# Optimization experiments

Hardware: AMD Instinct MI355X
Metric: run time of the kernel (lower is better)

The kernel has to match this reference:

```python
import math
import jax, jax.numpy as jnp
import numpy as np

# MrLoRA ranks: halving from highest_rank = total_rank//2 = 32 down to 1
RANKS = [32, 16, 8, 4, 2, 1]
TOTAL_R = sum(RANKS)  # 63
LORA_ALPHA = 16.0
IN_F, OUT_F = 4096, 4096
BATCH, SEQ = 4, 2048


def setup_inputs() -> dict:
    key = jax.random.key(0)
    k0, k1, k2, k3 = jax.random.split(key, 4)
    x = jax.random.normal(k0, (BATCH, SEQ, IN_F), dtype=jnp.float32)
    # Base linear layer (nn.Linear weight is [out, in], plus bias)
    W_base = jax.random.normal(k1, (OUT_F, IN_F), dtype=jnp.float32) * 0.02
    b_base = jnp.zeros((OUT_F,), dtype=jnp.float32)
    # Concatenated per-rank LoRA weights: A rows stacked -> [TOTAL_R, IN_F],
    # B cols stacked -> [OUT_F, TOTAL_R]. Mathematically identical to the
    # per-rank ModuleDict since the branch outputs are summed.
    A = jax.random.normal(k2, (TOTAL_R, IN_F), dtype=jnp.float32) / math.sqrt(IN_F)
    B = jax.random.normal(k3, (OUT_F, TOTAL_R), dtype=jnp.float32) * 0.02
    alphas = jnp.ones((len(RANKS),), dtype=jnp.float32)
    # use_rslora=True -> scaling = alpha / sqrt(r)
    scalings = jnp.array([LORA_ALPHA / math.sqrt(r) for r in RANKS], dtype=jnp.float32)
    return {"x": x, "W_base": W_base, "b_base": b_base, "A": A, "B": B,
            "alphas": alphas, "scalings": scalings}


def reference(x, W_base, b_base, A, B, alphas, scalings):
    # static map: row r of concatenated A belongs to which rank branch
    seg = np.repeat(np.arange(len(RANKS)), RANKS)  # [TOTAL_R]
    base = jnp.einsum('bsi,oi->bso', x, W_base) + b_base
    # dropout p=0 -> identity
    combined = (alphas * scalings)[seg]            # [TOTAL_R]
    z = jnp.einsum('bsi,ri->bsr', x, A) * combined # scaled low-rank projections
    adapter = jnp.einsum('bsr,or->bso', z, B)      # sum over all rank branches
    return base + adapter
```

## Files before the change

### kernel.cpp

```cpp
#include <hip/hip_runtime.h>
#include <hip/hip_fp16.h>
#include <cstdint>

#define IN_F 4096
#define OUT_F 4096
#define M_TOT 8192
#define TOTAL_R 63

typedef __attribute__((ext_vector_type(8))) _Float16 f16x8;
typedef __attribute__((ext_vector_type(4))) float f32x4;
typedef __attribute__((ext_vector_type(8))) unsigned short u16x8;
typedef __attribute__((ext_vector_type(4))) unsigned short u16x4;

__device__ __forceinline__ void gload_lds16(const void* g, void* l) {
  __builtin_amdgcn_global_load_lds((const __attribute__((address_space(1))) void*)g,
                                   (__attribute__((address_space(3))) void*)l,
                                   16, 0, 0);
}

__device__ __forceinline__ int seg_of(int r) {
  return (r < 32) ? 0 : (r < 48) ? 1 : (r < 56) ? 2 : (r < 60) ? 3 : (r < 62) ? 4 : 5;
}

__global__ __launch_bounds__(256) void prep_kernel(
    const float* __restrict__ x, const float* __restrict__ Wb,
    const float* __restrict__ A, const float* __restrict__ Bm,
    const float* __restrict__ alphas, const float* __restrict__ scalings,
    uint16_t* __restrict__ xh, uint16_t* __restrict__ wh) {
  __shared__ float sA[63 * 128];
  __shared__ float sCS[64];
  const int id = blockIdx.x;
  const int q9 = id / 9, rem = id % 9;
  const int t = threadIdx.x;

  if (rem != 8) {
    const int cid = q9 * 8 + rem;
    size_t i = (size_t)cid * 256 + t;
    const float4* xv = (const float4*)x;
    float4 v0 = xv[2 * i];
    float4 v1 = xv[2 * i + 1];
    float v[8] = {v0.x, v0.y, v0.z, v0.w, v1.x, v1.y, v1.z, v1.w};
    u16x8 h;
#pragma unroll
    for (int k = 0; k < 8; ++k) h[k] = __half_as_ushort(__float2half_rn(v[k]));
    *(u16x8*)(xh + 8 * i) = h;
    return;
  }

  const int mid = q9;
  const int o0 = (mid >> 5) * 64, i0 = (mid & 31) * 128;

  if (t < 64) {
    int r = t;
    sCS[t] = (r < TOTAL_R) ? alphas[seg_of(r)] * scalings[seg_of(r)] : 0.f;
  }
#pragma unroll
  for (int k = 0; k < 8; ++k) {
    int idx = k * 256 + t;
    if (idx < 63 * 32) {
      int r = idx >> 5, c = idx & 31;
      *(f32x4*)(sA + r * 128 + c * 4) =
          *(const f32x4*)(A + (size_t)r * IN_F + i0 + c * 4);
    }
  }
  __syncthreads();

  const int oo = t & 63, iq = t >> 6;
  const size_t ob = (size_t)(o0 + oo);
  const size_t obase = ob * IN_F + i0 + iq * 32;
  const float* bmrow = Bm + ob * TOTAL_R;
  f32x4 acc4[8];
#pragma unroll
  for (int v = 0; v < 8; ++v) acc4[v] = *(const f32x4*)(Wb + obase + v * 4);
#pragma unroll 9
  for (int r = 0; r < TOTAL_R; ++r) {
    const float coeff = bmrow[r] * sCS[r];
    const f32x4* ar = (const f32x4*)(sA + r * 128 + iq * 32);
#pragma unroll
    for (int v = 0; v < 8; ++v) acc4[v] += coeff * ar[v];
  }
#pragma unroll
  for (int v = 0; v < 8; ++v) {
    u16x4 h;
#pragma unroll
    for (int k = 0; k < 4; ++k) h[k] = __half_as_ushort(__float2half_rn(acc4[v][k]));
    *(u16x4*)(wh + obase + v * 4) = h;
  }
}

__global__ __launch_bounds__(512, 2) void gemm_mrlora(
    const uint16_t* __restrict__ xh, const uint16_t* __restrict__ wh,
    const float* __restrict__ bias, float* __restrict__ out) {
  __shared__ uint16_t lds[2][2][2][8192];
  const int t = threadIdx.x;
  const int l = t & 63;
  const int w = t >> 6;
  const int wm = w >> 2, wn = w & 3;
  const int lr = l & 15, lg = l >> 4;

  const int xcd = blockIdx.x & 7;
  const int kk = blockIdx.x >> 3;
  const int bm = xcd * 4 + (kk & 3);
  const int bn = kk >> 2;
  const size_t brow = (size_t)bm * 256;
  const size_t bcol = (size_t)bn * 256;

  const int sp = (t & 7) ^ ((t >> 3) & 7);
  const int grow = (t >> 3) * 2 + (sp >> 2);
  const int gcol = (sp & 3) * 8;
  const uint16_t* pX = xh + (brow + grow) * (size_t)IN_F + gcol;
  const uint16_t* pW = wh + (bcol + grow) * (size_t)IN_F + gcol;
  const int t8 = t * 8;

  int aoff[2][4], boff[4];
#pragma unroll
  for (int ih = 0; ih < 2; ++ih)
#pragma unroll
    for (int i2 = 0; i2 < 4; ++i2) {
      int row = wm * 128 + ih * 64 + i2 * 16 + lr;
      aoff[ih][i2] = (row >> 1) * 64 + (((((row & 1) << 2) | lg) ^ ((row >> 1) & 7)) << 3);
    }
#pragma unroll
  for (int j = 0; j < 4; ++j) {
    int row = wn * 64 + j * 16 + lr;
    boff[j] = (row >> 1) * 64 + (((((row & 1) << 2) | lg) ^ ((row >> 1) & 7)) << 3);
  }

  f32x4 acc[8][4] = {};
  f16x8 afr[4], bfr[4];

#define STG(NB, MAT, KS, KT)                                                   \
  do {                                                                         \
    const uint16_t* _s = ((MAT) ? pW : pX) + (KT) * 64 + (KS) * 32;            \
    gload_lds16(_s, &lds[NB][MAT][KS][t8]);                                    \
    gload_lds16(_s + 128 * (size_t)IN_F, &lds[NB][MAT][KS][t8 + 4096]);        \
  } while (0)

#define RDA(BUF, IH, KS)                                                       \
  _Pragma("unroll") for (int _i = 0; _i < 4; ++_i)                             \
      afr[_i] = *(const f16x8*)&lds[BUF][0][KS][aoff[IH][_i]];

#define RDB(BUF, KS)                                                           \
  _Pragma("unroll") for (int _j = 0; _j < 4; ++_j)                             \
      bfr[_j] = *(const f16x8*)&lds[BUF][1][KS][boff[_j]];

#define MM16(IH, KS)                                                           \
  do {                                                                         \
    __builtin_amdgcn_s_setprio(1);                                             \
    _Pragma("unroll") for (int _i = 0; _i < 4; ++_i)                           \
        _Pragma("unroll") for (int _j = 0; _j < 4; ++_j)                       \
            acc[(IH) * 4 + _i][_j] = __builtin_amdgcn_mfma_f32_16x16x32_f16(   \
                afr[_i], bfr[_j], acc[(IH) * 4 + _i][_j], 0, 0, 0);            \
    __builtin_amdgcn_s_setprio(0);                                             \
  } while (0)

#define BAR __builtin_amdgcn_s_barrier()

#define KTILE(BUF, KT, S2W, S4W, DOSTG)                                        \
  do {                                                                         \
                                                      \
    RDA(BUF, 0, 0); RDB(BUF, 0);                                               \
    if (DOSTG) STG(1 - (BUF), 0, 0, (KT) + 1);                                 \
    BAR;                                                                       \
    MM16(0, 0);                                                                \
    BAR;                                                                       \
                                             \
    RDA(BUF, 1, 0);                                                            \
    if (DOSTG) STG(1 - (BUF), 1, 0, (KT) + 1);                                 \
    BAR;                                                                       \
    MM16(1, 0);                                                                \
    asm volatile("s_waitcnt " S2W ::: "memory");  \
    BAR;                                                                       \
                                                      \
    RDA(BUF, 0, 1); RDB(BUF, 1);                                               \
    if (DOSTG) STG(1 - (BUF), 0, 1, (KT) + 1);                                 \
    BAR;                                                                       \
    MM16(0, 1);                                                                \
    BAR;                                                                       \
                                             \
    RDA(BUF, 1, 1);                                                            \
    if (DOSTG) STG(1 - (BUF), 1, 1, (KT) + 1);                                 \
    BAR;                                                                       \
    MM16(1, 1);                                                                \
    asm volatile("s_waitcnt " S4W ::: "memory");       \
    BAR;                                                                       \
  } while (0)

  STG(0, 0, 0, 0); STG(0, 1, 0, 0); STG(0, 0, 1, 0); STG(0, 1, 1, 0);
  asm volatile("s_waitcnt vmcnt(4)" ::: "memory");
  BAR;

#pragma unroll 1
  for (int tt = 0; tt < 31; ++tt) {
    KTILE(0, 2 * tt,     "vmcnt(4)", "vmcnt(4)", 1);
    KTILE(1, 2 * tt + 1, "vmcnt(4)", "vmcnt(4)", 1);
  }
  KTILE(0, 62, "vmcnt(4)", "vmcnt(4)", 1);
  KTILE(1, 63, "vmcnt(0)", "vmcnt(0)", 0);

#undef KTILE
#undef BAR
#undef MM16
#undef RDB
#undef RDA
#undef STG

#pragma unroll
  for (int j = 0; j < 4; ++j) {
    const size_t col = bcol + wn * 64 + j * 16 + lr;
    const float bs = bias[col];
#pragma unroll
    for (int i = 0; i < 8; ++i) {
      const size_t row0 = brow + wm * 128 + i * 16 + lg * 4;
#pragma unroll
      for (int r = 0; r < 4; ++r)
        out[(row0 + r) * OUT_F + col] = acc[i][j][r] + bs;
    }
  }
}


__global__ __launch_bounds__(256) void fb_z_kernel(const float* __restrict__ x,
                                                   const float* __restrict__ A,
                                                   const float* __restrict__ alphas,
                                                   const float* __restrict__ scalings,
                                                   float* __restrict__ z) {
  __shared__ float sx[IN_F];
  __shared__ float red[256];
  const int m = blockIdx.x, t = threadIdx.x;
  for (int i = t; i < IN_F / 4; i += 256)
    ((float4*)sx)[i] = ((const float4*)(x + (size_t)m * IN_F))[i];
  __syncthreads();
  const int r = t >> 2, q = t & 3;
  float part = 0.f;
  if (r < TOTAL_R) {
    const float4* Ar = (const float4*)(A + (size_t)r * IN_F + q * 1024);
    const float4* xs = (const float4*)(sx + q * 1024);
    for (int k = 0; k < 256; ++k) {
      float4 av = Ar[k], xv = xs[k];
      part += av.x * xv.x + av.y * xv.y + av.z * xv.z + av.w * xv.w;
    }
  }
  red[t] = part;
  __syncthreads();
  if (q == 0 && r < TOTAL_R) {
    int s = seg_of(r);
    z[(size_t)m * TOTAL_R + r] =
        alphas[s] * scalings[s] * (red[t] + red[t + 1] + red[t + 2] + red[t + 3]);
  }
}

__global__ __launch_bounds__(256) void fb_gemm_fp32(const float* __restrict__ x,
                                                    const float* __restrict__ Wb,
                                                    const float* __restrict__ bb,
                                                    const float* __restrict__ Bm,
                                                    const float* __restrict__ z,
                                                    float* __restrict__ out) {
  __shared__ float sx[64][33];
  __shared__ float sw[64][33];
  const int t = threadIdx.x;
  const int tr = t >> 4, tc = t & 15;
  const int bm = blockIdx.x / (OUT_F / 64);
  const int bn = blockIdx.x % (OUT_F / 64);
  const size_t brow = (size_t)bm * 64, bcol = (size_t)bn * 64;
  const int r = t >> 2, c0 = (t & 3) * 8;
  float acc[4][4] = {};
  for (int k0 = 0; k0 < IN_F; k0 += 32) {
    float4 a0 = *(const float4*)(x + (brow + r) * IN_F + k0 + c0);
    float4 a1 = *(const float4*)(x + (brow + r) * IN_F + k0 + c0 + 4);
    float4 w0 = *(const float4*)(Wb + (bcol + r) * IN_F + k0 + c0);
    float4 w1 = *(const float4*)(Wb + (bcol + r) * IN_F + k0 + c0 + 4);
    __syncthreads();
    sx[r][c0 + 0] = a0.x; sx[r][c0 + 1] = a0.y; sx[r][c0 + 2] = a0.z; sx[r][c0 + 3] = a0.w;
    sx[r][c0 + 4] = a1.x; sx[r][c0 + 5] = a1.y; sx[r][c0 + 6] = a1.z; sx[r][c0 + 7] = a1.w;
    sw[r][c0 + 0] = w0.x; sw[r][c0 + 1] = w0.y; sw[r][c0 + 2] = w0.z; sw[r][c0 + 3] = w0.w;
    sw[r][c0 + 4] = w1.x; sw[r][c0 + 5] = w1.y; sw[r][c0 + 6] = w1.z; sw[r][c0 + 7] = w1.w;
    __syncthreads();
#pragma unroll
    for (int k = 0; k < 32; ++k) {
      float xa[4], wv[4];
#pragma unroll
      for (int i = 0; i < 4; ++i) xa[i] = sx[tr + 16 * i][k];
#pragma unroll
      for (int j = 0; j < 4; ++j) wv[j] = sw[tc + 16 * j][k];
#pragma unroll
      for (int i = 0; i < 4; ++i)
#pragma unroll
        for (int j = 0; j < 4; ++j) acc[i][j] += xa[i] * wv[j];
    }
  }
#pragma unroll 1
  for (int rr = 0; rr < TOTAL_R; ++rr) {
    float zr[4], br[4];
#pragma unroll
    for (int i = 0; i < 4; ++i) zr[i] = z[(brow + tr + 16 * i) * TOTAL_R + rr];
#pragma unroll
    for (int j = 0; j < 4; ++j) br[j] = Bm[(bcol + tc + 16 * j) * TOTAL_R + rr];
#pragma unroll
    for (int i = 0; i < 4; ++i)
#pragma unroll
      for (int j = 0; j < 4; ++j) acc[i][j] += zr[i] * br[j];
  }
#pragma unroll
  for (int i = 0; i < 4; ++i)
#pragma unroll
    for (int j = 0; j < 4; ++j) {
      size_t row = brow + tr + 16 * i, col = bcol + tc + 16 * j;
      out[row * OUT_F + col] = acc[i][j] + bb[col];
    }
}

extern "C" void kernel_launch(void* const* d_in, const int* in_sizes, int n_in,
                              void* d_out, int out_size, void* d_ws, size_t ws_size,
                              hipStream_t stream) {
  const float* x  = (const float*)d_in[0];
  const float* Wb = (const float*)d_in[1];
  const float* bb = (const float*)d_in[2];
  const float* A  = (const float*)d_in[3];
  const float* Bm = (const float*)d_in[4];
  const float* al = (const float*)d_in[5];
  const float* sc = (const float*)d_in[6];
  float* out = (float*)d_out;

  const size_t MB = (size_t)1 << 20;
  if (ws_size >= 96 * MB) {
    char* ws = (char*)d_ws;
    uint16_t* xh = (uint16_t*)(ws);
    uint16_t* wh = (uint16_t*)(ws + 64 * MB);
    prep_kernel<<<18432, 256, 0, stream>>>(x, Wb, A, Bm, al, sc, xh, wh);
    gemm_mrlora<<<(M_TOT / 256) * (OUT_F / 256), 512, 0, stream>>>(xh, wh, bb, out);
  } else {
    float* z = (float*)d_ws;
    fb_z_kernel<<<M_TOT, 256, 0, stream>>>(x, A, al, sc, z);
    fb_gemm_fp32<<<(M_TOT / 64) * (OUT_F / 64), 256, 0, stream>>>(x, Wb, bb, Bm, z, out);
  }
}
```

Before: 337.0 us.

## Restructure GEMM K-loop into 4-stage LDS ring with 3-tile prefetch depth

Result: slower. 356.4 us (+5.8%).

```diff
diff --git a/kernel.cpp b/kernel.cpp
--- a/kernel.cpp
+++ b/kernel.cpp
@@ -91,7 +91,7 @@
 __global__ __launch_bounds__(512, 2) void gemm_mrlora(
     const uint16_t* __restrict__ xh, const uint16_t* __restrict__ wh,
     const float* __restrict__ bias, float* __restrict__ out) {
-  __shared__ uint16_t lds[2][2][2][8192];
+  __shared__ uint16_t lds[4][2][8192];
   const int t = threadIdx.x;
   const int l = t & 63;
   const int w = t >> 6;
@@ -129,22 +129,29 @@
   f32x4 acc[8][4] = {};
   f16x8 afr[4], bfr[4];
 
-#define STG(NB, MAT, KS, KT)                                                   \
+#define STGA(NB, KT)                                                           \
   do {                                                                         \
-    const uint16_t* _s = ((MAT) ? pW : pX) + (KT) * 64 + (KS) * 32;            \
-    gload_lds16(_s, &lds[NB][MAT][KS][t8]);                                    \
-    gload_lds16(_s + 128 * (size_t)IN_F, &lds[NB][MAT][KS][t8 + 4096]);        \
+    const uint16_t* _s = pX + (KT) * 32;                                       \
+    gload_lds16(_s, &lds[NB][0][t8]);                                          \
+    gload_lds16(_s + 128 * (size_t)IN_F, &lds[NB][0][t8 + 4096]);              \
   } while (0)
 
-#define RDA(BUF, IH, KS)                                                       \
+#define STGB(NB, KT)                                                           \
+  do {                                                                         \
+    const uint16_t* _s = pW + (KT) * 32;                                       \
+    gload_lds16(_s, &lds[NB][1][t8]);                                          \
+    gload_lds16(_s + 128 * (size_t)IN_F, &lds[NB][1][t8 + 4096]);              \
+  } while (0)
+
+#define RDA(BUF, IH)                                                           \
   _Pragma("unroll") for (int _i = 0; _i < 4; ++_i)                             \
-      afr[_i] = *(const f16x8*)&lds[BUF][0][KS][aoff[IH][_i]];
-
-#define RDB(BUF, KS)                                                           \
+      afr[_i] = *(const f16x8*)&lds[BUF][0][aoff[IH][_i]];
+
+#define RDB(BUF)                                                               \
   _Pragma("unroll") for (int _j = 0; _j < 4; ++_j)                             \
-      bfr[_j] = *(const f16x8*)&lds[BUF][1][KS][boff[_j]];
-
-#define MM16(IH, KS)                                                           \
+      bfr[_j] = *(const f16x8*)&lds[BUF][1][boff[_j]];
+
+#define MM16(IH)                                                               \
   do {                                                                         \
     __builtin_amdgcn_s_setprio(1);                                             \
     _Pragma("unroll") for (int _i = 0; _i < 4; ++_i)                           \
@@ -156,54 +163,40 @@
 
 #define BAR __builtin_amdgcn_s_barrier()
 
-#define KTILE(BUF, KT, S2W, S4W, DOSTG)                                        \
-  do {                                                                         \
-                                                      \
-    RDA(BUF, 0, 0); RDB(BUF, 0);                                               \
-    if (DOSTG) STG(1 - (BUF), 0, 0, (KT) + 1);                                 \
-    BAR;                                                                       \
-    MM16(0, 0);                                                                \
-    BAR;                                                                       \
-                                             \
-    RDA(BUF, 1, 0);                                                            \
-    if (DOSTG) STG(1 - (BUF), 1, 0, (KT) + 1);                                 \
-    BAR;                                                                       \
-    MM16(1, 0);                                                                \
-    asm volatile("s_waitcnt " S2W ::: "memory");  \
-    BAR;                                                                       \
-                                                      \
-    RDA(BUF, 0, 1); RDB(BUF, 1);                                               \
-    if (DOSTG) STG(1 - (BUF), 0, 1, (KT) + 1);                                 \
-    BAR;                                                                       \
-    MM16(0, 1);                                                                \
-    BAR;                                                                       \
-                                             \
-    RDA(BUF, 1, 1);                                                            \
-    if (DOSTG) STG(1 - (BUF), 1, 1, (KT) + 1);                                 \
-    BAR;                                                                       \
-    MM16(1, 1);                                                                \
-    asm volatile("s_waitcnt " S4W ::: "memory");       \
-    BAR;                                                                       \
-  } while (0)
-
-  STG(0, 0, 0, 0); STG(0, 1, 0, 0); STG(0, 0, 1, 0); STG(0, 1, 1, 0);
-  asm volatile("s_waitcnt vmcnt(4)" ::: "memory");
+  STGA(0, 0); STGB(0, 0);
+  STGA(1, 1); STGB(1, 1);
+  STGA(2, 2); STGB(2, 2);
+  asm volatile("s_waitcnt vmcnt(8)" ::: "memory");
   BAR;
 
 #pragma unroll 1
-  for (int tt = 0; tt < 31; ++tt) {
-    KTILE(0, 2 * tt,     "vmcnt(4)", "vmcnt(4)", 1);
-    KTILE(1, 2 * tt + 1, "vmcnt(4)", "vmcnt(4)", 1);
-  }
-  KTILE(0, 62, "vmcnt(4)", "vmcnt(4)", 1);
-  KTILE(1, 63, "vmcnt(0)", "vmcnt(0)", 0);
-
-#undef KTILE
+  for (int kt = 0; kt < 128; ++kt) {
+    const int cb = kt & 3;
+    RDA(cb, 0); RDB(cb);
+    if (kt <= 124) STGA((kt + 3) & 3, kt + 3);
+    BAR;
+    MM16(0);
+    BAR;
+    RDA(cb, 1);
+    if (kt <= 124) STGB((kt + 3) & 3, kt + 3);
+    BAR;
+    MM16(1);
+    if (kt <= 124) {
+      asm volatile("s_waitcnt vmcnt(8)" ::: "memory");
+    } else if (kt == 125) {
+      asm volatile("s_waitcnt vmcnt(4)" ::: "memory");
+    } else if (kt == 126) {
+      asm volatile("s_waitcnt vmcnt(0)" ::: "memory");
+    }
+    BAR;
+  }
+
 #undef BAR
 #undef MM16
 #undef RDB
 #undef RDA
-#undef STG
+#undef STGB
+#undef STGA
 
 #pragma unroll
   for (int j = 0; j < 4; ++j) {
```
